# Performance work log

Measured on AMD Instinct MI355X. Metric: run time of the kernel, lower is better.

The kernel has to match this reference:

```python
import jax, jax.numpy as jnp
import numpy as np

N_TYPES = 4
N_DESC = 8
K_MAX = 8
R_C = 5.0
L_MAX = 4
N_ATOMS = 10000
M_NBR = 20


def chebyshev_basis(r, r_c, k_max):
    fc = jnp.where(r < r_c, 0.5 * jnp.cos(jnp.pi * r / r_c) + 0.5, jnp.zeros_like(r))
    x = 2.0 * (r / r_c - 1.0) ** 2 - 1.0
    fn = [jnp.ones_like(x), x]
    for _ in range(2, k_max):
        fn.append(2.0 * x * fn[-1] - fn[-2])
    fn = jnp.stack(fn[:k_max], axis=-1)  # [T, k_max]
    return (fn + 1.0) * (0.5 * fc)[..., None]


def legendre_basis(cos_theta, l_max):
    pl = [jnp.ones_like(cos_theta), cos_theta]
    for l in range(2, l_max):
        pl.append(((2 * l - 1) * cos_theta * pl[-1] - (l - 1) * pl[-2]) / l)
    return jnp.stack(pl[:l_max], axis=-1)  # [T, l_max]


def setup_inputs() -> dict:
    key = jax.random.key(0)
    k1, k2, k3, k4 = jax.random.split(key, 4)
    types = jax.random.randint(k1, (N_ATOMS,), 0, N_TYPES)
    # small box so pair distances mostly fall under the cutoff r_c
    positions = jax.random.uniform(k2, (N_ATOMS, 3), dtype=jnp.float32) * 4.0
    # all neighbor slots valid (no -1 padding) and never the atom itself
    offs = jax.random.randint(k3, (N_ATOMS, M_NBR), 1, N_ATOMS)
    angular_neighbors = (jnp.arange(N_ATOMS)[:, None] + offs) % N_ATOMS
    c_table = jax.random.normal(k4, (N_TYPES, N_TYPES, N_DESC, K_MAX), dtype=jnp.float32)
    return {"types": types, "positions": positions,
            "angular_neighbors": angular_neighbors, "c_table": c_table}


def reference(types, positions, angular_neighbors, c_table):
    N, M = angular_neighbors.shape
    ju, ku = np.triu_indices(M, 1)  # P = M*(M-1)//2 pairs per atom
    P = ju.shape[0]
    j_idx = angular_neighbors[:, ju].reshape(-1)  # [N*P]
    k_idx = angular_neighbors[:, ku].reshape(-1)
    i_idx = jnp.repeat(jnp.arange(N), P)

    pos_i = positions[i_idx]
    rij = positions[j_idx] - pos_i
    rik = positions[k_idx] - pos_i
    r_ij = jnp.linalg.norm(rij, axis=-1)
    r_ik = jnp.linalg.norm(rik, axis=-1)
    cos_theta = jnp.sum(rij * rik, axis=-1) / (r_ij * r_ik + 1e-8)

    type_i = types[i_idx]
    f_ij = chebyshev_basis(r_ij, R_C, K_MAX)  # [T, k]
    f_ik = chebyshev_basis(r_ik, R_C, K_MAX)
    c_ij = c_table[type_i, types[j_idx]]  # [T, n_desc, k]
    c_ik = c_table[type_i, types[k_idx]]
    g_ij = jnp.einsum('tdk,tk->td', c_ij, f_ij)  # [T, n_desc]
    g_ik = jnp.einsum('tdk,tk->td', c_ik, f_ik)

    P_l = legendre_basis(cos_theta, L_MAX)  # [T, l_max]
    ang = (g_ij * g_ik)[:, :, None] * P_l[:, None, :]  # [T, n_desc, l_max]
    q = jax.ops.segment_sum(ang, i_idx, num_segments=N)  # [N, n_desc, l_max]
    return q
```

## Files before the change

kernel.cpp:

```cpp
#include <hip/hip_runtime.h>

#define N_TYPES 4
#define N_DESC  8
#define K_MAX   8
#define L_MAX   4
#define M_NBR   20
#define NPAIR   (M_NBR * (M_NBR - 1) / 2)
#define ATOMS_PER_BLOCK 4

constexpr float R_C = 5.0f;
constexpr float PI_F = 3.14159265358979323846f;

__global__ __launch_bounds__(256) void AngularDescriptor_kernel(
    const int*   __restrict__ types,
    const float* __restrict__ pos,
    const int*   __restrict__ nbr,
    const float* __restrict__ c_table,
    float*       __restrict__ out,
    int N)
{
    __shared__ float4 sd4[ATOMS_PER_BLOCK][M_NBR];
    __shared__ float  sf [ATOMS_PER_BLOCK][M_NBR][K_MAX];
    __shared__ float  sg [ATOMS_PER_BLOCK][M_NBR][N_DESC];
    __shared__ int    stj[ATOMS_PER_BLOCK][M_NBR];
    __shared__ unsigned short spair[NPAIR];

    const int t    = threadIdx.x;
    const int w    = t >> 6;
    const int lane = t & 63;
    const int atom = blockIdx.x * ATOMS_PER_BLOCK + w;

    if (t < NPAIR) {
        int rem = t, m1 = 0;
        while (rem >= M_NBR - 1 - m1) { rem -= M_NBR - 1 - m1; ++m1; }
        spair[t] = (unsigned short)((m1 << 5) | (m1 + 1 + rem));
    }

    float px = 0.f, py = 0.f, pz = 0.f;
    int ti = 0;
    if (atom < N) {
        ti = types[atom];
        px = pos[atom * 3 + 0];
        py = pos[atom * 3 + 1];
        pz = pos[atom * 3 + 2];
    }

    if (atom < N && lane < M_NBR) {
        const int j = nbr[atom * M_NBR + lane];
        const float dx = pos[j * 3 + 0] - px;
        const float dy = pos[j * 3 + 1] - py;
        const float dz = pos[j * 3 + 2] - pz;
        const float r  = sqrtf(dx * dx + dy * dy + dz * dz);
        sd4[w][lane] = make_float4(dx, dy, dz, r);
        stj[w][lane] = types[j];

        const float fc  = (r < R_C) ? (0.5f * cosf(PI_F * r / R_C) + 0.5f) : 0.0f;
        const float hfc = 0.5f * fc;
        const float u   = r / R_C - 1.0f;
        const float x   = 2.0f * u * u - 1.0f;
        float tkm2 = 1.0f, tkm1 = x;
        sf[w][lane][0] = 2.0f * hfc;
        sf[w][lane][1] = (x + 1.0f) * hfc;
        #pragma unroll
        for (int k = 2; k < K_MAX; ++k) {
            const float tk = 2.0f * x * tkm1 - tkm2;
            sf[w][lane][k] = (tk + 1.0f) * hfc;
            tkm2 = tkm1; tkm1 = tk;
        }
    }
    __syncthreads();

    const int d = lane & 7;
    const int g = lane >> 3;

    if (atom < N) {
        for (int m = g; m < M_NBR; m += 8) {
            const int tj = stj[w][m];
            const float* c = c_table + (((ti * N_TYPES + tj) * N_DESC + d) * K_MAX);
            const float4 c0 = ((const float4*)c)[0];
            const float4 c1 = ((const float4*)c)[1];
            const float* f = sf[w][m];
            const float acc = c0.x * f[0] + c0.y * f[1] + c0.z * f[2] + c0.w * f[3]
                            + c1.x * f[4] + c1.y * f[5] + c1.z * f[6] + c1.w * f[7];
            sg[w][m][d] = acc;
        }
    }
    __syncthreads();

    float a0 = 0.f, a1 = 0.f, a2 = 0.f, a3 = 0.f;
    if (atom < N) {
        for (int p = g; p < NPAIR; p += 8) {
            const int pe = spair[p];
            const int m1 = pe >> 5, m2 = pe & 31;
            const float4 v1 = sd4[w][m1];
            const float4 v2 = sd4[w][m2];
            const float dot   = v1.x * v2.x + v1.y * v2.y + v1.z * v2.z;
            const float denom = v1.w * v2.w + 1e-8f;
            const float c  = dot * __builtin_amdgcn_rcpf(denom);
            const float gg = sg[w][m1][d] * sg[w][m2][d];
            const float P2 = 1.5f * c * c - 0.5f;
            const float P3 = (5.0f * c * P2 - 2.0f * c) * (1.0f / 3.0f);
            a0 += gg;
            a1 = fmaf(gg, c,  a1);
            a2 = fmaf(gg, P2, a2);
            a3 = fmaf(gg, P3, a3);
        }
    }

    #pragma unroll
    for (int off = 8; off <= 32; off <<= 1) {
        a0 += __shfl_xor(a0, off, 64);
        a1 += __shfl_xor(a1, off, 64);
        a2 += __shfl_xor(a2, off, 64);
        a3 += __shfl_xor(a3, off, 64);
    }

    if (atom < N && lane < 8) {
        ((float4*)out)[atom * N_DESC + d] = make_float4(a0, a1, a2, a3);
    }
}

extern "C" void kernel_launch(void* const* d_in, const int* in_sizes, int n_in,
                              void* d_out, int out_size, void* d_ws, size_t ws_size,
                              hipStream_t stream) {
    const int*   types   = (const int*)  d_in[0];
    const float* pos     = (const float*)d_in[1];
    const int*   nbr     = (const int*)  d_in[2];
    const float* c_table = (const float*)d_in[3];
    float*       out     = (float*)      d_out;

    const int N = in_sizes[0];
    const int grid = (N + ATOMS_PER_BLOCK - 1) / ATOMS_PER_BLOCK;
    AngularDescriptor_kernel<<<grid, 256, 0, stream>>>(types, pos, nbr, c_table, out, N);
}
```

Measured before the change: 74.25 us.

## Replace pairwise angular loop with Legendre addition-theorem moment decomposition

Replaces the O(M^2) loop over neighbor pairs with a factorization based on the spherical-harmonic addition theorem. Each neighbor contributes 20 Cartesian harmonic components up to degree 3, and the pair sums are recovered from squared weighted moments minus the diagonal term. This removes the per-pair reciprocal and Legendre evaluation and cuts arithmetic per atom from 190 pairs to 20 neighbors by 20 components. It also switches to fast rsq/cos intrinsics. The trade-off is that the 1e-8 epsilon in the denominator is dropped and summation order changes, so rounding differs slightly.

```diff
diff --git a/kernel.cpp b/kernel.cpp
--- a/kernel.cpp
+++ b/kernel.cpp
@@ -5,11 +5,13 @@
 #define K_MAX   8
 #define L_MAX   4
 #define M_NBR   20
-#define NPAIR   (M_NBR * (M_NBR - 1) / 2)
+#define NCOMP   20
 #define ATOMS_PER_BLOCK 4
 
-constexpr float R_C = 5.0f;
-constexpr float PI_F = 3.14159265358979323846f;
+constexpr float R_C  = 5.0f;
+constexpr float SQ2  = 1.41421356237309515f;
+constexpr float SQ3  = 1.73205080756887729f;
+constexpr float SQ6  = 2.44948974968163702f;
 
 __global__ __launch_bounds__(256) void AngularDescriptor_kernel(
     const int*   __restrict__ types,
@@ -19,22 +21,15 @@
     float*       __restrict__ out,
     int N)
 {
-    __shared__ float4 sd4[ATOMS_PER_BLOCK][M_NBR];
-    __shared__ float  sf [ATOMS_PER_BLOCK][M_NBR][K_MAX];
-    __shared__ float  sg [ATOMS_PER_BLOCK][M_NBR][N_DESC];
-    __shared__ int    stj[ATOMS_PER_BLOCK][M_NBR];
-    __shared__ unsigned short spair[NPAIR];
+    __shared__ float sfeat[ATOMS_PER_BLOCK][NCOMP][M_NBR];
+    __shared__ float scheb[ATOMS_PER_BLOCK][M_NBR][K_MAX];
+    __shared__ float sg   [ATOMS_PER_BLOCK][N_DESC][M_NBR];
+    __shared__ int   stj  [ATOMS_PER_BLOCK][M_NBR];
 
     const int t    = threadIdx.x;
     const int w    = t >> 6;
     const int lane = t & 63;
     const int atom = blockIdx.x * ATOMS_PER_BLOCK + w;
-
-    if (t < NPAIR) {
-        int rem = t, m1 = 0;
-        while (rem >= M_NBR - 1 - m1) { rem -= M_NBR - 1 - m1; ++m1; }
-        spair[t] = (unsigned short)((m1 << 5) | (m1 + 1 + rem));
-    }
 
     float px = 0.f, py = 0.f, pz = 0.f;
     int ti = 0;
@@ -50,73 +45,120 @@
         const float dx = pos[j * 3 + 0] - px;
         const float dy = pos[j * 3 + 1] - py;
         const float dz = pos[j * 3 + 2] - pz;
-        const float r  = sqrtf(dx * dx + dy * dy + dz * dz);
-        sd4[w][lane] = make_float4(dx, dy, dz, r);
-        stj[w][lane] = types[j];
+        const float r2   = dx * dx + dy * dy + dz * dz;
+        const float rinv = __builtin_amdgcn_rsqf(r2);
+        const float r    = r2 * rinv;
 
-        const float fc  = (r < R_C) ? (0.5f * cosf(PI_F * r / R_C) + 0.5f) : 0.0f;
+        const float fc  = (r < R_C) ? (0.5f * __builtin_amdgcn_cosf(r * (0.5f / R_C)) + 0.5f)
+                                    : 0.0f;
         const float hfc = 0.5f * fc;
-        const float u   = r / R_C - 1.0f;
+        const float u   = r * (1.0f / R_C) - 1.0f;
         const float x   = 2.0f * u * u - 1.0f;
+        float ch[K_MAX];
+        ch[0] = 2.0f * hfc;
+        ch[1] = (x + 1.0f) * hfc;
         float tkm2 = 1.0f, tkm1 = x;
-        sf[w][lane][0] = 2.0f * hfc;
-        sf[w][lane][1] = (x + 1.0f) * hfc;
         #pragma unroll
         for (int k = 2; k < K_MAX; ++k) {
             const float tk = 2.0f * x * tkm1 - tkm2;
-            sf[w][lane][k] = (tk + 1.0f) * hfc;
+            ch[k] = (tk + 1.0f) * hfc;
             tkm2 = tkm1; tkm1 = tk;
+        }
+        ((float4*)&scheb[w][lane][0])[0] = make_float4(ch[0], ch[1], ch[2], ch[3]);
+        ((float4*)&scheb[w][lane][0])[1] = make_float4(ch[4], ch[5], ch[6], ch[7]);
+        stj[w][lane] = types[j];
+
+        const float ux = dx * rinv, uy = dy * rinv, uz = dz * rinv;
+        const float x2 = ux * ux, y2 = uy * uy, z2 = uz * uz;
+        float F[NCOMP];
+        F[0]  = 1.0f;
+        F[1]  = ux;  F[2] = uy;  F[3] = uz;
+        F[4]  = x2 - (1.0f / 3.0f);
+        F[5]  = y2 - (1.0f / 3.0f);
+        F[6]  = z2 - (1.0f / 3.0f);
+        F[7]  = SQ2 * ux * uy;
+        F[8]  = SQ2 * ux * uz;
+        F[9]  = SQ2 * uy * uz;
+        F[10] = ux * (x2 - 0.6f);
+        F[11] = uy * (y2 - 0.6f);
+        F[12] = uz * (z2 - 0.6f);
+        F[13] = SQ3 * uy * (x2 - 0.2f);
+        F[14] = SQ3 * uz * (x2 - 0.2f);
+        F[15] = SQ3 * ux * (y2 - 0.2f);
+        F[16] = SQ3 * uz * (y2 - 0.2f);
+        F[17] = SQ3 * ux * (z2 - 0.2f);
+        F[18] = SQ3 * uy * (z2 - 0.2f);
+        F[19] = SQ6 * ux * uy * uz;
+        #pragma unroll
+        for (int c = 0; c < NCOMP; ++c) sfeat[w][c][lane] = F[c];
+    }
+    __syncthreads();
+
+    const int d  = lane & 7;
+    const int gp = lane >> 3;
+
+    if (atom < N) {
+        #pragma unroll
+        for (int m = gp; m < M_NBR; m += 8) {
+            const int tj = stj[w][m];
+            const float* c = c_table + (((ti * N_TYPES + tj) * N_DESC + d) * K_MAX);
+            const float4 c0 = ((const float4*)c)[0];
+            const float4 c1 = ((const float4*)c)[1];
+            const float4 f0 = ((const float4*)&scheb[w][m][0])[0];
+            const float4 f1 = ((const float4*)&scheb[w][m][0])[1];
+            sg[w][d][m] = c0.x * f0.x + c0.y * f0.y + c0.z * f0.z + c0.w * f0.w
+                        + c1.x * f1.x + c1.y * f1.y + c1.z * f1.z + c1.w * f1.w;
         }
     }
     __syncthreads();
 
-    const int d = lane & 7;
-    const int g = lane >> 3;
+    float p0 = 0.f, p1 = 0.f, p2 = 0.f, p3 = 0.f;
+    float hG2 = 0.f;
+    if (atom < N) {
+        float g[M_NBR];
+        #pragma unroll
+        for (int i = 0; i < 5; ++i) {
+            const float4 v = ((const float4*)&sg[w][d][0])[i];
+            g[4*i+0] = v.x; g[4*i+1] = v.y; g[4*i+2] = v.z; g[4*i+3] = v.w;
+        }
+        float G2 = 0.f;
+        #pragma unroll
+        for (int m = 0; m < M_NBR; ++m) G2 = fmaf(g[m], g[m], G2);
+        hG2 = 0.5f * G2;
 
-    if (atom < N) {
-        for (int m = g; m < M_NBR; m += 8) {
-            const int tj = stj[w][m];
-            const float* c = c_table + (((ti * N_TYPES + tj) * N_DESC + d) * K_MAX);
-            const float4 c0 = ((const float4*)c)[0];
-            const float4 c1 = ((const float4*)c)[1];
-            const float* f = sf[w][m];
-            const float acc = c0.x * f[0] + c0.y * f[1] + c0.z * f[2] + c0.w * f[3]
-                            + c1.x * f[4] + c1.y * f[5] + c1.z * f[6] + c1.w * f[7];
-            sg[w][m][d] = acc;
-        }
-    }
-    __syncthreads();
-
-    float a0 = 0.f, a1 = 0.f, a2 = 0.f, a3 = 0.f;
-    if (atom < N) {
-        for (int p = g; p < NPAIR; p += 8) {
-            const int pe = spair[p];
-            const int m1 = pe >> 5, m2 = pe & 31;
-            const float4 v1 = sd4[w][m1];
-            const float4 v2 = sd4[w][m2];
-            const float dot   = v1.x * v2.x + v1.y * v2.y + v1.z * v2.z;
-            const float denom = v1.w * v2.w + 1e-8f;
-            const float c  = dot * __builtin_amdgcn_rcpf(denom);
-            const float gg = sg[w][m1][d] * sg[w][m2][d];
-            const float P2 = 1.5f * c * c - 0.5f;
-            const float P3 = (5.0f * c * P2 - 2.0f * c) * (1.0f / 3.0f);
-            a0 += gg;
-            a1 = fmaf(gg, c,  a1);
-            a2 = fmaf(gg, P2, a2);
-            a3 = fmaf(gg, P3, a3);
+        #pragma unroll
+        for (int s = 0; s < 3; ++s) {
+            const int c = gp + 8 * s;
+            if (c < NCOMP) {
+                float acc = 0.f;
+                #pragma unroll
+                for (int i = 0; i < 5; ++i) {
+                    const float4 v = ((const float4*)&sfeat[w][c][0])[i];
+                    acc = fmaf(g[4*i+0], v.x, acc);
+                    acc = fmaf(g[4*i+1], v.y, acc);
+                    acc = fmaf(g[4*i+2], v.z, acc);
+                    acc = fmaf(g[4*i+3], v.w, acc);
+                }
+                const float v2 = acc * acc;
+                if      (c == 0)  p0 += 0.50f * v2;
+                else if (c <= 3)  p1 += 0.50f * v2;
+                else if (c <= 9)  p2 += 0.75f * v2;
+                else              p3 += 1.25f * v2;
+            }
         }
     }
 
     #pragma unroll
     for (int off = 8; off <= 32; off <<= 1) {
-        a0 += __shfl_xor(a0, off, 64);
-        a1 += __shfl_xor(a1, off, 64);
-        a2 += __shfl_xor(a2, off, 64);
-        a3 += __shfl_xor(a3, off, 64);
+        p0 += __shfl_xor(p0, off, 64);
+        p1 += __shfl_xor(p1, off, 64);
+        p2 += __shfl_xor(p2, off, 64);
+        p3 += __shfl_xor(p3, off, 64);
     }
 
     if (atom < N && lane < 8) {
-        ((float4*)out)[atom * N_DESC + d] = make_float4(a0, a1, a2, a3);
+        ((float4*)out)[atom * N_DESC + d] =
+            make_float4(p0 - hG2, p1 - hG2, p2 - hG2, p3 - hG2);
     }
 }
 
```

After: 66.08 us. -11.0%, faster.
